# Kernel optimization log

Hardware: AMD Instinct MI355X
Metric: run time of the kernel (lower is better)

## Reference

```python
import jax, jax.numpy as jnp
import numpy as np

N = 50000        # nodes
E = 800_000      # edges (avg degree 16)
D_IN, D_HID, D_OUT = 512, 512, 256
P_DROP = 0.5


def setup_inputs() -> dict:
    key = jax.random.key(0)
    k0, k1, k2, k3 = jax.random.split(key, 4)
    x = jax.random.normal(k0, (N, D_IN), dtype=jnp.float32)
    edge_index = jax.random.randint(k1, (2, E), 0, N, dtype=jnp.int64)
    W1 = jax.random.normal(k2, (D_HID, D_IN), dtype=jnp.float32) * 0.02
    b1 = jnp.zeros((D_HID,), dtype=jnp.float32)
    W2 = jax.random.normal(k3, (D_OUT, D_HID), dtype=jnp.float32) * 0.02
    b2 = jnp.zeros((D_OUT,), dtype=jnp.float32)
    return {"x": x, "edge_index": edge_index, "W1": W1, "b1": b1, "W2": W2, "b2": b2}


def _gcn_norm(edge_index, n):
    # add self loops, then symmetric GCN normalization: D^-1/2 (A+I) D^-1/2
    src, dst = edge_index[0], edge_index[1]
    loops = jnp.arange(n, dtype=src.dtype)
    src = jnp.concatenate([src, loops])
    dst = jnp.concatenate([dst, loops])
    deg = jax.ops.segment_sum(jnp.ones_like(src, dtype=jnp.float32), dst, num_segments=n)
    dinv = jax.lax.rsqrt(deg)  # deg >= 1 because of self loops
    norm = dinv[src] * dinv[dst]  # [E+N]
    return src, dst, norm


def _propagate(x, src, dst, norm):
    # out[i] = sum_{(j->i)} norm_e * x[j]
    return jax.ops.segment_sum(x[src] * norm[:, None], dst, num_segments=x.shape[0])


def reference(x, edge_index, W1, b1, W2, b2):
    src, dst, norm = _gcn_norm(edge_index, x.shape[0])
    # SGConv layer 1 (K=1): propagate then linear
    h = _propagate(x, src, dst, norm) @ W1.T + b1
    h = jax.nn.relu(h)
    # F.dropout(p) with training=True default -> deterministic fixed-key mask here
    keep = jax.random.bernoulli(jax.random.key(42), 1.0 - P_DROP, h.shape)
    embedding = jnp.where(keep, h / (1.0 - P_DROP), 0.0)
    # SGConv layer 2
    out = _propagate(embedding, src, dst, norm) @ W2.T + b2
    return embedding, out
```

## Files before the change

kernel.cpp:

```cpp
#include <hip/hip_runtime.h>

typedef unsigned short u16t;
typedef __attribute__((ext_vector_type(8))) short short8;
typedef __attribute__((ext_vector_type(4))) short short4v;
typedef __attribute__((ext_vector_type(4))) float f32x4;
typedef __attribute__((ext_vector_type(4))) unsigned short u16x4;

__device__ __forceinline__ float bf2f(short b) {
  return __uint_as_float(((unsigned)(unsigned short)b) << 16);
}
__device__ __forceinline__ u16t f2bf(float f) {
  unsigned u = __float_as_uint(f);
  u += 0x7FFFu + ((u >> 16) & 1u);
  return (u16t)(u >> 16);
}

__device__ __forceinline__ bool keep_mask(unsigned flat) {
  const unsigned k0 = 0u, k1 = 42u;
  const unsigned k2 = k0 ^ k1 ^ 0x1BD11BDAu;
  unsigned x0 = 0u + k0;
  unsigned x1 = flat + k1;
#define TF_R(r) { x0 += x1; x1 = (x1 << r) | (x1 >> (32 - r)); x1 ^= x0; }
  TF_R(13) TF_R(15) TF_R(26) TF_R(6)  x0 += k1; x1 += k2 + 1u;
  TF_R(17) TF_R(29) TF_R(16) TF_R(24) x0 += k2; x1 += k0 + 2u;
  TF_R(13) TF_R(15) TF_R(26) TF_R(6)  x0 += k0; x1 += k1 + 3u;
  TF_R(17) TF_R(29) TF_R(16) TF_R(24) x0 += k1; x1 += k2 + 4u;
  TF_R(13) TF_R(15) TF_R(26) TF_R(6)  x0 += k2; x1 += k0 + 5u;
#undef TF_R
  return ((x0 ^ x1) >> 31) == 0u;
}

__device__ __forceinline__ void load_lds16(const u16t* g, u16t* l) {
  __builtin_amdgcn_global_load_lds((__attribute__((address_space(1))) void*)g,
                                   (__attribute__((address_space(3))) void*)l,
                                   16, 0, 0);
}

__global__ void cvt_bf16(const float* __restrict__ s, u16t* __restrict__ d, int n) {
  int i = (blockIdx.x * 256 + threadIdx.x) * 4;
  if (i < n) {
    f32x4 v = *(const f32x4*)&s[i];
    u16x4 o = { f2bf(v.x), f2bf(v.y), f2bf(v.z), f2bf(v.w) };
    *(u16x4*)&d[i] = o;
  }
}

__global__ void count_edges(const int* __restrict__ dst, int E, int* __restrict__ cnt) {
  int e = blockIdx.x * 256 + threadIdx.x;
  if (e < E) atomicAdd(&cnt[dst[e]], 1);
}

__global__ __launch_bounds__(256) void rowp_build(const int* __restrict__ cnt,
    int* __restrict__ rowp, int* __restrict__ cursor, float* __restrict__ dinv,
    int* __restrict__ gctr, int n) {
  __shared__ int sd[256];
  __shared__ int sbase;
  const int tid = threadIdx.x;
  const int i = blockIdx.x * 256 + tid;
  int c = (i < n) ? cnt[i] : 0;
  int v = c;
  sd[tid] = v;
  __syncthreads();
  for (int o = 1; o < 256; o <<= 1) {
    int t = (tid >= o) ? sd[tid - o] : 0;
    __syncthreads();
    v += t;
    sd[tid] = v;
    __syncthreads();
  }
  if (tid == 255) sbase = atomicAdd(gctr, v);
  __syncthreads();
  if (i < n) {
    int start = sbase + v - c;
    rowp[i] = start;
    cursor[i] = start;
    dinv[i] = rsqrtf((float)(c + 1));
  }
}

__global__ void fill_csr(const int* __restrict__ src, const int* __restrict__ dst, int E,
                         int* __restrict__ cursor, int* __restrict__ col) {
  int e = blockIdx.x * 256 + threadIdx.x;
  if (e < E) {
    int d = dst[e];
    int pos = atomicAdd(&cursor[d], 1);
    col[pos] = src[e];
  }
}

__global__ __launch_bounds__(256) void gemm_bt(const u16t* __restrict__ A,
                                               const u16t* __restrict__ B,
                                               u16t* __restrict__ C,
                                               int K, int Ncols) {
  __shared__ __align__(16) u16t lA[128 * 32];
  __shared__ __align__(16) u16t lB[128 * 32];
  const int tid = threadIdx.x;
  const int wave = tid >> 6, lane = tid & 63;
  const int wm = (wave & 1) * 64, wn = (wave >> 1) * 64;
  const int lrow = lane & 15, lq = lane >> 4;
  const u16t* Ab = A + (size_t)blockIdx.x * 128 * K;
  const u16t* Bb = B + (size_t)blockIdx.y * 128 * K;
  const int r0 = tid >> 2, c0 = (tid & 3) * 8;
  const int ldsOff = __builtin_amdgcn_readfirstlane((tid >> 6) * 512);

  f32x4 acc[4][4];
  const f32x4 zero = {0.f, 0.f, 0.f, 0.f};
#pragma unroll
  for (int mi = 0; mi < 4; ++mi)
#pragma unroll
    for (int ni = 0; ni < 4; ++ni) acc[mi][ni] = zero;

  for (int kt = 0; kt < K; kt += 32) {
    __syncthreads();
    load_lds16(Ab + (size_t)r0 * K + kt + c0, &lA[ldsOff]);
    load_lds16(Ab + (size_t)(r0 + 64) * K + kt + c0, &lA[2048 + ldsOff]);
    load_lds16(Bb + (size_t)r0 * K + kt + c0, &lB[ldsOff]);
    load_lds16(Bb + (size_t)(r0 + 64) * K + kt + c0, &lB[2048 + ldsOff]);
    __syncthreads();
    short8 af[4], bfr[4];
#pragma unroll
    for (int mi = 0; mi < 4; ++mi)
      af[mi] = *(const short8*)&lA[(wm + mi * 16 + lrow) * 32 + lq * 8];
#pragma unroll
    for (int ni = 0; ni < 4; ++ni)
      bfr[ni] = *(const short8*)&lB[(wn + ni * 16 + lrow) * 32 + lq * 8];
#pragma unroll
    for (int mi = 0; mi < 4; ++mi)
#pragma unroll
      for (int ni = 0; ni < 4; ++ni)
        acc[mi][ni] = __builtin_amdgcn_mfma_f32_16x16x32_bf16(af[mi], bfr[ni], acc[mi][ni], 0, 0, 0);
  }

  const size_t crow = (size_t)blockIdx.x * 128 + wm + lq * 4;
  const int ccol = blockIdx.y * 128 + wn + lrow;
#pragma unroll
  for (int mi = 0; mi < 4; ++mi)
#pragma unroll
    for (int r = 0; r < 4; ++r)
#pragma unroll
      for (int ni = 0; ni < 4; ++ni)
        C[(crow + mi * 16 + r) * Ncols + ccol + ni * 16] = f2bf(acc[mi][ni][r]);
}

__global__ __launch_bounds__(256) void prop1_kernel(const u16t* __restrict__ y1,
    const int* __restrict__ col, const int* __restrict__ rowp, const int* __restrict__ rowend,
    const float* __restrict__ dinv, const float* __restrict__ b1,
    float* __restrict__ embf, u16t* __restrict__ embb, int n) {
  const int lane = threadIdx.x & 63;
  const int i = blockIdx.x * 4 + (threadIdx.x >> 6);
  if (i >= n) return;
  const int f = lane * 8;
  const float di = dinv[i];
  float acc[8];
  short8 v = *(const short8*)&y1[(size_t)i * 512 + f];
#pragma unroll
  for (int j = 0; j < 8; ++j) acc[j] = di * bf2f(v[j]);
  int e = rowp[i];
  const int e1 = rowend[i];
  for (; e + 4 <= e1; e += 4) {
    const int s0 = col[e], s1 = col[e + 1], s2 = col[e + 2], s3 = col[e + 3];
    const float w0 = dinv[s0], w1 = dinv[s1], w2 = dinv[s2], w3 = dinv[s3];
    short8 u0 = *(const short8*)&y1[(size_t)s0 * 512 + f];
    short8 u1 = *(const short8*)&y1[(size_t)s1 * 512 + f];
    short8 u2 = *(const short8*)&y1[(size_t)s2 * 512 + f];
    short8 u3 = *(const short8*)&y1[(size_t)s3 * 512 + f];
#pragma unroll
    for (int j = 0; j < 8; ++j) acc[j] += w0 * bf2f(u0[j]);
#pragma unroll
    for (int j = 0; j < 8; ++j) acc[j] += w1 * bf2f(u1[j]);
#pragma unroll
    for (int j = 0; j < 8; ++j) acc[j] += w2 * bf2f(u2[j]);
#pragma unroll
    for (int j = 0; j < 8; ++j) acc[j] += w3 * bf2f(u3[j]);
  }
  for (; e < e1; ++e) {
    const int s = col[e];
    const float w = dinv[s];
    short8 u = *(const short8*)&y1[(size_t)s * 512 + f];
#pragma unroll
    for (int j = 0; j < 8; ++j) acc[j] += w * bf2f(u[j]);
  }
  const unsigned flat = (unsigned)i * 512u + (unsigned)f;
  f32x4 o0, o1;
  short8 ob;
#pragma unroll
  for (int j = 0; j < 8; ++j) {
    float h = di * acc[j] + b1[f + j];
    h = fmaxf(h, 0.f);
    float eb = keep_mask(flat + (unsigned)j) ? 2.f * h : 0.f;
    if (j < 4) o0[j] = eb; else o1[j - 4] = eb;
    ob[j] = (short)f2bf(eb);
  }
  *(f32x4*)&embf[(size_t)i * 512 + f] = o0;
  *(f32x4*)&embf[(size_t)i * 512 + f + 4] = o1;
  *(short8*)&embb[(size_t)i * 512 + f] = ob;
}

__global__ __launch_bounds__(256) void prop2_kernel(const u16t* __restrict__ z,
    const int* __restrict__ col, const int* __restrict__ rowp, const int* __restrict__ rowend,
    const float* __restrict__ dinv, const float* __restrict__ b2,
    float* __restrict__ outp, int n) {
  const int lane = threadIdx.x & 63;
  const int i = blockIdx.x * 4 + (threadIdx.x >> 6);
  if (i >= n) return;
  const int f = lane * 4;
  const float di = dinv[i];
  float acc[4];
  short4v v = *(const short4v*)&z[(size_t)i * 256 + f];
#pragma unroll
  for (int j = 0; j < 4; ++j) acc[j] = di * bf2f(v[j]);
  int e = rowp[i];
  const int e1 = rowend[i];
  for (; e + 4 <= e1; e += 4) {
    const int s0 = col[e], s1 = col[e + 1], s2 = col[e + 2], s3 = col[e + 3];
    const float w0 = dinv[s0], w1 = dinv[s1], w2 = dinv[s2], w3 = dinv[s3];
    short4v u0 = *(const short4v*)&z[(size_t)s0 * 256 + f];
    short4v u1 = *(const short4v*)&z[(size_t)s1 * 256 + f];
    short4v u2 = *(const short4v*)&z[(size_t)s2 * 256 + f];
    short4v u3 = *(const short4v*)&z[(size_t)s3 * 256 + f];
#pragma unroll
    for (int j = 0; j < 4; ++j) acc[j] += w0 * bf2f(u0[j]);
#pragma unroll
    for (int j = 0; j < 4; ++j) acc[j] += w1 * bf2f(u1[j]);
#pragma unroll
    for (int j = 0; j < 4; ++j) acc[j] += w2 * bf2f(u2[j]);
#pragma unroll
    for (int j = 0; j < 4; ++j) acc[j] += w3 * bf2f(u3[j]);
  }
  for (; e < e1; ++e) {
    const int s = col[e];
    const float w = dinv[s];
    short4v u = *(const short4v*)&z[(size_t)s * 256 + f];
#pragma unroll
    for (int j = 0; j < 4; ++j) acc[j] += w * bf2f(u[j]);
  }
  f32x4 o;
#pragma unroll
  for (int j = 0; j < 4; ++j) o[j] = di * acc[j] + b2[f + j];
  *(f32x4*)&outp[(size_t)i * 256 + f] = o;
}

extern "C" void kernel_launch(void* const* d_in, const int* in_sizes, int n_in,
                              void* d_out, int out_size, void* d_ws, size_t ws_size,
                              hipStream_t stream) {
  (void)n_in; (void)out_size; (void)ws_size;
  const float* x  = (const float*)d_in[0];
  const int*   ei = (const int*)d_in[1];
  const float* W1 = (const float*)d_in[2];
  const float* b1 = (const float*)d_in[3];
  const float* W2 = (const float*)d_in[4];
  const float* b2 = (const float*)d_in[5];

  const int Nn = in_sizes[0] / 512;
  const int E  = in_sizes[1] / 2;
  const int Mpad = ((Nn + 127) / 128) * 128;
  const int K = 512;

  char* ws = (char*)d_ws;
  size_t off = 0;
  auto take = [&](size_t bytes) -> char* {
    char* p = ws + off;
    off += (bytes + 255) & ~(size_t)255;
    return p;
  };
  u16t* xb   = (u16t*)take((size_t)Mpad * 512 * 2);
  u16t* y1b  = (u16t*)take((size_t)Mpad * 512 * 2);
  u16t* W1b  = (u16t*)take((size_t)512 * 512 * 2);
  u16t* W2b  = (u16t*)take((size_t)256 * 512 * 2);
  int*   cnt    = (int*)take((size_t)(Nn + 1) * 4);
  int*   rowp   = (int*)take((size_t)Nn * 4);
  int*   cursor = (int*)take((size_t)Nn * 4);
  float* dinv   = (float*)take((size_t)Nn * 4);
  int*   colA   = (int*)take((size_t)E * 4);

  float* embf = (float*)d_out;
  float* outf = (float*)d_out + (size_t)Nn * 512;

  hipMemsetAsync(cnt, 0, (size_t)(Nn + 1) * 4, stream);

  const int n1 = Nn * 512;
  cvt_bf16<<<(n1 / 4 + 255) / 256, 256, 0, stream>>>(x, xb, n1);
  cvt_bf16<<<(512 * 512 / 4 + 255) / 256, 256, 0, stream>>>(W1, W1b, 512 * 512);
  cvt_bf16<<<(256 * 512 / 4 + 255) / 256, 256, 0, stream>>>(W2, W2b, 256 * 512);

  count_edges<<<(E + 255) / 256, 256, 0, stream>>>(ei + E, E, cnt);
  rowp_build<<<(Nn + 255) / 256, 256, 0, stream>>>(cnt, rowp, cursor, dinv, cnt + Nn, Nn);
  fill_csr<<<(E + 255) / 256, 256, 0, stream>>>(ei, ei + E, E, cursor, colA);

  dim3 g1(Mpad / 128, 4);
  gemm_bt<<<g1, 256, 0, stream>>>(xb, W1b, y1b, K, 512);
  prop1_kernel<<<(Nn + 3) / 4, 256, 0, stream>>>(y1b, colA, rowp, cursor, dinv, b1,
                                                 embf, xb , Nn);

  u16t* zb = y1b;
  dim3 g2(Mpad / 128, 2);
  gemm_bt<<<g2, 256, 0, stream>>>(xb, W2b, zb, K, 256);
  prop2_kernel<<<(Nn + 3) / 4, 256, 0, stream>>>(zb, colA, rowp, cursor, dinv, b2, outf, Nn);
}
```

Baseline: 592.7 us.

## Slice GEMM outputs into 32-column panels and precompute dropout bitmask

The GEMM now writes its output as 16 (or 8) column panels of 32 features each, laid out node-major within a panel. The propagation kernels assign blocks to one panel at a time, so the neighbour gathers touch a smaller working set that can stay in cache. Column indices are stored as 16-bit values, which only works for node counts below 65536. The dropout mask is computed once as a bitmask inside the x conversion kernel instead of running Threefry per element in prop1, and output writes use nontemporal stores. The cost is more blocks per propagation pass and a graph-size limit.

```diff
diff --git a/kernel.cpp b/kernel.cpp
--- a/kernel.cpp
+++ b/kernel.cpp
@@ -42,6 +42,23 @@
     f32x4 v = *(const f32x4*)&s[i];
     u16x4 o = { f2bf(v.x), f2bf(v.y), f2bf(v.z), f2bf(v.w) };
     *(u16x4*)&d[i] = o;
+  }
+}
+
+__global__ __launch_bounds__(256) void cvt_x_mask(const float* __restrict__ s,
+    u16t* __restrict__ d, unsigned* __restrict__ mask, int n, int nwords) {
+  int t = blockIdx.x * 256 + threadIdx.x;
+  int i = t * 4;
+  if (i < n) {
+    f32x4 v = *(const f32x4*)&s[i];
+    u16x4 o = { f2bf(v.x), f2bf(v.y), f2bf(v.z), f2bf(v.w) };
+    *(u16x4*)&d[i] = o;
+  }
+  if (t < nwords) {
+    unsigned base = (unsigned)t * 32u;
+    unsigned m = 0u;
+    for (int k = 0; k < 32; ++k) m |= (keep_mask(base + (unsigned)k) ? 1u : 0u) << k;
+    mask[t] = m;
   }
 }
 
@@ -79,19 +96,19 @@
 }
 
 __global__ void fill_csr(const int* __restrict__ src, const int* __restrict__ dst, int E,
-                         int* __restrict__ cursor, int* __restrict__ col) {
+                         int* __restrict__ cursor, u16t* __restrict__ col) {
   int e = blockIdx.x * 256 + threadIdx.x;
   if (e < E) {
     int d = dst[e];
     int pos = atomicAdd(&cursor[d], 1);
-    col[pos] = src[e];
-  }
-}
-
-__global__ __launch_bounds__(256) void gemm_bt(const u16t* __restrict__ A,
-                                               const u16t* __restrict__ B,
-                                               u16t* __restrict__ C,
-                                               int K, int Ncols) {
+    col[pos] = (u16t)src[e];
+  }
+}
+
+__global__ __launch_bounds__(256) void gemm_bt_sl(const u16t* __restrict__ A,
+                                                  const u16t* __restrict__ B,
+                                                  u16t* __restrict__ C,
+                                                  int K, int Mrows) {
   __shared__ __align__(16) u16t lA[128 * 32];
   __shared__ __align__(16) u16t lB[128 * 32];
   const int tid = threadIdx.x;
@@ -131,93 +148,116 @@
         acc[mi][ni] = __builtin_amdgcn_mfma_f32_16x16x32_bf16(af[mi], bfr[ni], acc[mi][ni], 0, 0, 0);
   }
 
-  const size_t crow = (size_t)blockIdx.x * 128 + wm + lq * 4;
-  const int ccol = blockIdx.y * 128 + wn + lrow;
+  const int crow0 = blockIdx.x * 128 + wm + lq * 4;
+  const int ccol0 = blockIdx.y * 128 + wn + lrow;
 #pragma unroll
   for (int mi = 0; mi < 4; ++mi)
 #pragma unroll
     for (int r = 0; r < 4; ++r)
 #pragma unroll
-      for (int ni = 0; ni < 4; ++ni)
-        C[(crow + mi * 16 + r) * Ncols + ccol + ni * 16] = f2bf(acc[mi][ni][r]);
-}
-
-__global__ __launch_bounds__(256) void prop1_kernel(const u16t* __restrict__ y1,
-    const int* __restrict__ col, const int* __restrict__ rowp, const int* __restrict__ rowend,
+      for (int ni = 0; ni < 4; ++ni) {
+        int cc = ccol0 + ni * 16;
+        size_t idx = ((size_t)(cc >> 5) * Mrows + (crow0 + mi * 16 + r)) * 32 + (cc & 31);
+        C[idx] = f2bf(acc[mi][ni][r]);
+      }
+}
+
+__global__ __launch_bounds__(256) void prop1_kernel(const u16t* __restrict__ y1s,
+    const u16t* __restrict__ colu, const int* __restrict__ rowp, const int* __restrict__ rowend,
     const float* __restrict__ dinv, const float* __restrict__ b1,
-    float* __restrict__ embf, u16t* __restrict__ embb, int n) {
-  const int lane = threadIdx.x & 63;
-  const int i = blockIdx.x * 4 + (threadIdx.x >> 6);
+    const unsigned* __restrict__ kmask,
+    float* __restrict__ embf, u16t* __restrict__ embb, int n, int Mrows, int chunks) {
+  const int t = threadIdx.x;
+  const int fl4 = (t & 7) * 4;
+  const int bid = blockIdx.x;
+  const int half = chunks << 3;
+  const int phase = bid >= half;
+  const int rem = bid - (phase ? half : 0);
+  const int sl = (rem & 7) + (phase << 3);
+  const int i = (rem >> 3) * 32 + (t >> 3);
   if (i >= n) return;
-  const int f = lane * 8;
+
+  const u16t* T = y1s + (size_t)sl * Mrows * 32;
   const float di = dinv[i];
-  float acc[8];
-  short8 v = *(const short8*)&y1[(size_t)i * 512 + f];
-#pragma unroll
-  for (int j = 0; j < 8; ++j) acc[j] = di * bf2f(v[j]);
+  float acc[4];
+  {
+    short4v u = *(const short4v*)&T[(size_t)i * 32 + fl4];
+#pragma unroll
+    for (int j = 0; j < 4; ++j) acc[j] = di * bf2f(u[j]);
+  }
   int e = rowp[i];
   const int e1 = rowend[i];
   for (; e + 4 <= e1; e += 4) {
-    const int s0 = col[e], s1 = col[e + 1], s2 = col[e + 2], s3 = col[e + 3];
+    const int s0 = (int)colu[e], s1 = (int)colu[e + 1];
+    const int s2 = (int)colu[e + 2], s3 = (int)colu[e + 3];
     const float w0 = dinv[s0], w1 = dinv[s1], w2 = dinv[s2], w3 = dinv[s3];
-    short8 u0 = *(const short8*)&y1[(size_t)s0 * 512 + f];
-    short8 u1 = *(const short8*)&y1[(size_t)s1 * 512 + f];
-    short8 u2 = *(const short8*)&y1[(size_t)s2 * 512 + f];
-    short8 u3 = *(const short8*)&y1[(size_t)s3 * 512 + f];
-#pragma unroll
-    for (int j = 0; j < 8; ++j) acc[j] += w0 * bf2f(u0[j]);
-#pragma unroll
-    for (int j = 0; j < 8; ++j) acc[j] += w1 * bf2f(u1[j]);
-#pragma unroll
-    for (int j = 0; j < 8; ++j) acc[j] += w2 * bf2f(u2[j]);
-#pragma unroll
-    for (int j = 0; j < 8; ++j) acc[j] += w3 * bf2f(u3[j]);
+    short4v u0 = *(const short4v*)&T[(size_t)s0 * 32 + fl4];
+    short4v u1 = *(const short4v*)&T[(size_t)s1 * 32 + fl4];
+    short4v u2 = *(const short4v*)&T[(size_t)s2 * 32 + fl4];
+    short4v u3 = *(const short4v*)&T[(size_t)s3 * 32 + fl4];
+#pragma unroll
+    for (int j = 0; j < 4; ++j) acc[j] += w0 * bf2f(u0[j]);
+#pragma unroll
+    for (int j = 0; j < 4; ++j) acc[j] += w1 * bf2f(u1[j]);
+#pragma unroll
+    for (int j = 0; j < 4; ++j) acc[j] += w2 * bf2f(u2[j]);
+#pragma unroll
+    for (int j = 0; j < 4; ++j) acc[j] += w3 * bf2f(u3[j]);
   }
   for (; e < e1; ++e) {
-    const int s = col[e];
+    const int s = (int)colu[e];
     const float w = dinv[s];
-    short8 u = *(const short8*)&y1[(size_t)s * 512 + f];
-#pragma unroll
-    for (int j = 0; j < 8; ++j) acc[j] += w * bf2f(u[j]);
-  }
-  const unsigned flat = (unsigned)i * 512u + (unsigned)f;
-  f32x4 o0, o1;
-  short8 ob;
-#pragma unroll
-  for (int j = 0; j < 8; ++j) {
+    short4v u = *(const short4v*)&T[(size_t)s * 32 + fl4];
+#pragma unroll
+    for (int j = 0; j < 4; ++j) acc[j] += w * bf2f(u[j]);
+  }
+
+  const int f = sl * 32 + fl4;
+  const unsigned km = kmask[i * 16 + sl];
+  f32x4 o;
+  short4v ob;
+#pragma unroll
+  for (int j = 0; j < 4; ++j) {
     float h = di * acc[j] + b1[f + j];
     h = fmaxf(h, 0.f);
-    float eb = keep_mask(flat + (unsigned)j) ? 2.f * h : 0.f;
-    if (j < 4) o0[j] = eb; else o1[j - 4] = eb;
+    float eb = ((km >> (fl4 + j)) & 1u) ? 2.f * h : 0.f;
+    o[j] = eb;
     ob[j] = (short)f2bf(eb);
   }
-  *(f32x4*)&embf[(size_t)i * 512 + f] = o0;
-  *(f32x4*)&embf[(size_t)i * 512 + f + 4] = o1;
-  *(short8*)&embb[(size_t)i * 512 + f] = ob;
-}
-
-__global__ __launch_bounds__(256) void prop2_kernel(const u16t* __restrict__ z,
-    const int* __restrict__ col, const int* __restrict__ rowp, const int* __restrict__ rowend,
+  __builtin_nontemporal_store(o, (f32x4*)&embf[(size_t)i * 512 + f]);
+  __builtin_nontemporal_store(ob, (short4v*)&embb[(size_t)i * 512 + f]);
+}
+
+__global__ __launch_bounds__(256) void prop2_kernel(const u16t* __restrict__ zs,
+    const u16t* __restrict__ colu, const int* __restrict__ rowp, const int* __restrict__ rowend,
     const float* __restrict__ dinv, const float* __restrict__ b2,
-    float* __restrict__ outp, int n) {
-  const int lane = threadIdx.x & 63;
-  const int i = blockIdx.x * 4 + (threadIdx.x >> 6);
+    float* __restrict__ outp, int n, int Mrows, int chunks) {
+  const int t = threadIdx.x;
+  const int fl4 = (t & 7) * 4;
+  const int bid = blockIdx.x;
+  const int sl = bid & 7;
+  const int i = (bid >> 3) * 32 + (t >> 3);
+  (void)chunks;
   if (i >= n) return;
-  const int f = lane * 4;
+
+  const u16t* T = zs + (size_t)sl * Mrows * 32;
   const float di = dinv[i];
   float acc[4];
-  short4v v = *(const short4v*)&z[(size_t)i * 256 + f];
-#pragma unroll
-  for (int j = 0; j < 4; ++j) acc[j] = di * bf2f(v[j]);
+  {
+    short4v u = *(const short4v*)&T[(size_t)i * 32 + fl4];
+#pragma unroll
+    for (int j = 0; j < 4; ++j) acc[j] = di * bf2f(u[j]);
+  }
   int e = rowp[i];
   const int e1 = rowend[i];
   for (; e + 4 <= e1; e += 4) {
-    const int s0 = col[e], s1 = col[e + 1], s2 = col[e + 2], s3 = col[e + 3];
+    const int s0 = (int)colu[e], s1 = (int)colu[e + 1];
+    const int s2 = (int)colu[e + 2], s3 = (int)colu[e + 3];
     const float w0 = dinv[s0], w1 = dinv[s1], w2 = dinv[s2], w3 = dinv[s3];
-    short4v u0 = *(const short4v*)&z[(size_t)s0 * 256 + f];
-    short4v u1 = *(const short4v*)&z[(size_t)s1 * 256 + f];
-    short4v u2 = *(const short4v*)&z[(size_t)s2 * 256 + f];
-    short4v u3 = *(const short4v*)&z[(size_t)s3 * 256 + f];
+    short4v u0 = *(const short4v*)&T[(size_t)s0 * 32 + fl4];
+    short4v u1 = *(const short4v*)&T[(size_t)s1 * 32 + fl4];
+    short4v u2 = *(const short4v*)&T[(size_t)s2 * 32 + fl4];
+    short4v u3 = *(const short4v*)&T[(size_t)s3 * 32 + fl4];
 #pragma unroll
     for (int j = 0; j < 4; ++j) acc[j] += w0 * bf2f(u0[j]);
 #pragma unroll
@@ -228,16 +268,18 @@
     for (int j = 0; j < 4; ++j) acc[j] += w3 * bf2f(u3[j]);
   }
   for (; e < e1; ++e) {
-    const int s = col[e];
+    const int s = (int)colu[e];
     const float w = dinv[s];
-    short4v u = *(const short4v*)&z[(size_t)s * 256 + f];
+    short4v u = *(const short4v*)&T[(size_t)s * 32 + fl4];
 #pragma unroll
     for (int j = 0; j < 4; ++j) acc[j] += w * bf2f(u[j]);
   }
+
+  const int f = sl * 32 + fl4;
   f32x4 o;
 #pragma unroll
   for (int j = 0; j < 4; ++j) o[j] = di * acc[j] + b2[f + j];
-  *(f32x4*)&outp[(size_t)i * 256 + f] = o;
+  __builtin_nontemporal_store(o, (f32x4*)&outp[(size_t)i * 256 + f]);
 }
 
 extern "C" void kernel_launch(void* const* d_in, const int* in_sizes, int n_in,
@@ -255,6 +297,7 @@
   const int E  = in_sizes[1] / 2;
   const int Mpad = ((Nn + 127) / 128) * 128;
   const int K = 512;
+  const int CH = (Nn + 31) / 32;
 
   char* ws = (char*)d_ws;
   size_t off = 0;
@@ -264,14 +307,15 @@
     return p;
   };
   u16t* xb   = (u16t*)take((size_t)Mpad * 512 * 2);
-  u16t* y1b  = (u16t*)take((size_t)Mpad * 512 * 2);
+  u16t* y1s  = (u16t*)take((size_t)16 * Mpad * 32 * 2);
   u16t* W1b  = (u16t*)take((size_t)512 * 512 * 2);
   u16t* W2b  = (u16t*)take((size_t)256 * 512 * 2);
   int*   cnt    = (int*)take((size_t)(Nn + 1) * 4);
   int*   rowp   = (int*)take((size_t)Nn * 4);
   int*   cursor = (int*)take((size_t)Nn * 4);
   float* dinv   = (float*)take((size_t)Nn * 4);
-  int*   colA   = (int*)take((size_t)E * 4);
+  u16t*  colu   = (u16t*)take((size_t)E * 2);
+  unsigned* kmask = (unsigned*)take((size_t)Nn * 16 * 4);
 
   float* embf = (float*)d_out;
   float* outf = (float*)d_out + (size_t)Nn * 512;
@@ -279,21 +323,21 @@
   hipMemsetAsync(cnt, 0, (size_t)(Nn + 1) * 4, stream);
 
   const int n1 = Nn * 512;
-  cvt_bf16<<<(n1 / 4 + 255) / 256, 256, 0, stream>>>(x, xb, n1);
+  cvt_x_mask<<<(n1 / 4 + 255) / 256, 256, 0, stream>>>(x, xb, kmask, n1, Nn * 16);
   cvt_bf16<<<(512 * 512 / 4 + 255) / 256, 256, 0, stream>>>(W1, W1b, 512 * 512);
   cvt_bf16<<<(256 * 512 / 4 + 255) / 256, 256, 0, stream>>>(W2, W2b, 256 * 512);
 
   count_edges<<<(E + 255) / 256, 256, 0, stream>>>(ei + E, E, cnt);
   rowp_build<<<(Nn + 255) / 256, 256, 0, stream>>>(cnt, rowp, cursor, dinv, cnt + Nn, Nn);
-  fill_csr<<<(E + 255) / 256, 256, 0, stream>>>(ei, ei + E, E, cursor, colA);
+  fill_csr<<<(E + 255) / 256, 256, 0, stream>>>(ei, ei + E, E, cursor, colu);
 
   dim3 g1(Mpad / 128, 4);
-  gemm_bt<<<g1, 256, 0, stream>>>(xb, W1b, y1b, K, 512);
-  prop1_kernel<<<(Nn + 3) / 4, 256, 0, stream>>>(y1b, colA, rowp, cursor, dinv, b1,
-                                                 embf, xb , Nn);
-
-  u16t* zb = y1b;
+  gemm_bt_sl<<<g1, 256, 0, stream>>>(xb, W1b, y1s, K, Mpad);
+  prop1_kernel<<<16 * CH, 256, 0, stream>>>(y1s, colu, rowp, cursor, dinv, b1, kmask,
+                                            embf, xb , Nn, Mpad, CH);
+
+  u16t* zs = y1s;
   dim3 g2(Mpad / 128, 2);
-  gemm_bt<<<g2, 256, 0, stream>>>(xb, W2b, zb, K, 256);
-  prop2_kernel<<<(Nn + 3) / 4, 256, 0, stream>>>(zb, colA, rowp, cursor, dinv, b2, outf, Nn);
-}
+  gemm_bt_sl<<<g2, 256, 0, stream>>>(xb, W2b, zs, K, Mpad);
+  prop2_kernel<<<8 * CH, 256, 0, stream>>>(zs, colu, rowp, cursor, dinv, b2, outf, Nn, Mpad, CH);
+}
```

Result: slower. 664.4 us (+12.1%).
